# Kernel optimization log

Hardware: AMD Instinct MI355X
Metric: run time of the kernel (lower is better)

Reference implementation:

```python
import jax, jax.numpy as jnp
import numpy as np

EMBED_DIM = 1024
N_HEADS = 16
HEAD_DIM = EMBED_DIM // N_HEADS


def setup_inputs() -> dict:
    key = jax.random.key(0)
    k_x, k_wi, k_bi, k_wo, k_bo = jax.random.split(key, 5)
    B, N, C = 4, 2048, EMBED_DIM
    scale = 1.0 / np.sqrt(C)
    return {
        "x": jax.random.normal(k_x, (B, N, C), dtype=jnp.float32),
        "w_in": jax.random.normal(k_wi, (C, 3 * C), dtype=jnp.float32) * scale,
        "b_in": jax.random.normal(k_bi, (3 * C,), dtype=jnp.float32) * 0.01,
        "w_out": jax.random.normal(k_wo, (C, C), dtype=jnp.float32) * scale,
        "b_out": jax.random.normal(k_bo, (C,), dtype=jnp.float32) * 0.01,
    }


def reference(x, w_in, b_in, w_out, b_out):
    B, N, C = x.shape
    H, D = N_HEADS, HEAD_DIM
    qkv = x @ w_in + b_in  # (B, N, 3C)
    q, k, v = jnp.split(qkv, 3, axis=-1)
    # (B, H, N, D)
    q = q.reshape(B, N, H, D).transpose(0, 2, 1, 3)
    k = k.reshape(B, N, H, D).transpose(0, 2, 1, 3)
    v = v.reshape(B, N, H, D).transpose(0, 2, 1, 3)
    # Naive attention: full (B,H,N,N) scores, NO sqrt(d) scaling (as in source)
    scores = jnp.einsum("bhnd,bhmd->bhnm", q, k)
    attn = jax.nn.softmax(scores, axis=-1)
    out = jnp.einsum("bhnm,bhmd->bhnd", attn, v)
    out = out.transpose(0, 2, 1, 3).reshape(B, N, C)
    return out @ w_out + b_out
```

## Files before the change

### kernel.cpp

```cpp
#include <hip/hip_runtime.h>
#include <hip/hip_bf16.h>
#include <stdint.h>

typedef __attribute__((ext_vector_type(8))) __bf16 bf8v;
typedef __attribute__((ext_vector_type(4))) float f4v;

#define L2E 1.44269504088896f

__device__ __forceinline__ unsigned short f2bf(float f) {
  union { float f; unsigned u; } v; v.f = f;
  unsigned r = v.u + 0x7fffu + ((v.u >> 16) & 1u);
  return (unsigned short)(r >> 16);
}

__device__ __forceinline__ unsigned pk2bf(float f0, float f1) {
  union { __hip_bfloat162 h; unsigned u; } c;
  c.h = __float22bfloat162_rn(make_float2(f0, f1));
  return c.u;
}

__device__ __forceinline__ float exp2_hw(float x) {
  return __builtin_amdgcn_exp2f(x);
}

__device__ __forceinline__ void gl_lds16(const void* g, void* l) {
  __builtin_amdgcn_global_load_lds(
      (__attribute__((address_space(1))) void*)(g),
      (__attribute__((address_space(3))) void*)(l), 16, 0, 0);
}

__global__ void cast_bf16_kernel(const float* __restrict__ in,
                                 unsigned short* __restrict__ out) {
  int i = blockIdx.x * 256 + threadIdx.x;
  float4 v = ((const float4*)in)[i];
  ushort4 o;
  o.x = f2bf(v.x); o.y = f2bf(v.y); o.z = f2bf(v.z); o.w = f2bf(v.w);
  ((ushort4*)out)[i] = o;
}

__global__ void transpose_w_kernel(const float* __restrict__ w_in,
                                   const float* __restrict__ w_out,
                                   unsigned short* __restrict__ wiT,
                                   unsigned short* __restrict__ woT) {
  __shared__ float tile[32][33];
  int bx = blockIdx.x;
  const float* in; unsigned short* out; int C, c0;
  if (bx < 96) { in = w_in;  out = wiT; C = 3072; c0 = bx * 32; }
  else         { in = w_out; out = woT; C = 1024; c0 = (bx - 96) * 32; }
  int r0 = blockIdx.y * 32;
  int tx = threadIdx.x, ty = threadIdx.y;
#pragma unroll
  for (int j = 0; j < 4; ++j)
    tile[ty + 8 * j][tx] = in[(size_t)(r0 + ty + 8 * j) * C + c0 + tx];
  __syncthreads();
#pragma unroll
  for (int j = 0; j < 4; ++j)
    out[(size_t)(c0 + ty + 8 * j) * 1024 + r0 + tx] = f2bf(tile[tx][ty + 8 * j]);
}

__global__ void transpose_v_kernel(const unsigned short* __restrict__ qkv,
                                   unsigned short* __restrict__ vtg) {
  __shared__ unsigned short tile[32][33];
  int bh = blockIdx.z;
  int d0 = blockIdx.y * 32;
  int n0 = blockIdx.x * 32;
  int b = bh >> 4, h = bh & 15;
  int tx = threadIdx.x, ty = threadIdx.y;
  const unsigned short* src = qkv + (size_t)b * 2048 * 3072 + 2048 + h * 64 + d0;
#pragma unroll
  for (int j = 0; j < 4; ++j)
    tile[ty + 8 * j][tx] = src[(size_t)(n0 + ty + 8 * j) * 3072 + tx];
  __syncthreads();
  unsigned short* dst = vtg + ((size_t)bh * 64) * 2048;
#pragma unroll
  for (int j = 0; j < 4; ++j)
    dst[(size_t)(d0 + ty + 8 * j) * 2048 + n0 + tx] = tile[tx][ty + 8 * j];
}

__global__ __launch_bounds__(256, 2) void gemm_bt(
    const unsigned short* __restrict__ A,
    const unsigned short* __restrict__ BT,
    const float* __restrict__ bias,
    unsigned short* __restrict__ C,
    int M, int N, int K, int scale_ncols, float scale) {
  __shared__ __align__(16) unsigned short As[128 * 32];
  __shared__ __align__(16) unsigned short Bs[128 * 32];
  const int tid = threadIdx.x;
  const int wave = tid >> 6, lane = tid & 63;
  const int lo = lane & 15, hi = lane >> 4;
  const int m0 = blockIdx.y * 128, n0 = blockIdx.x * 128;
  const int wm = (wave >> 1) * 64, wn = (wave & 1) * 64;

  f4v acc[4][4] = {};

  const int srow = lane >> 2;
  const int scol = (lane & 3) * 8;

  for (int k0 = 0; k0 < K; k0 += 32) {
#pragma unroll
    for (int p = 0; p < 2; ++p) {
      int r = p * 64 + wave * 16 + srow;
      gl_lds16(A + (size_t)(m0 + r) * K + k0 + scol,
               &As[(p * 64 + wave * 16) * 32]);
      gl_lds16(BT + (size_t)(n0 + r) * K + k0 + scol,
               &Bs[(p * 64 + wave * 16) * 32]);
    }
    __syncthreads();
    bf8v a[4], b[4];
#pragma unroll
    for (int i = 0; i < 4; ++i)
      a[i] = *(const bf8v*)&As[(wm + i * 16 + lo) * 32 + hi * 8];
#pragma unroll
    for (int j = 0; j < 4; ++j)
      b[j] = *(const bf8v*)&Bs[(wn + j * 16 + lo) * 32 + hi * 8];
#pragma unroll
    for (int i = 0; i < 4; ++i)
#pragma unroll
      for (int j = 0; j < 4; ++j)
        acc[i][j] = __builtin_amdgcn_mfma_f32_16x16x32_bf16(a[i], b[j], acc[i][j], 0, 0, 0);
    __syncthreads();
  }

#pragma unroll
  for (int i = 0; i < 4; ++i) {
#pragma unroll
    for (int r = 0; r < 4; ++r) {
      int row = m0 + wm + i * 16 + hi * 4 + r;
#pragma unroll
      for (int j = 0; j < 4; ++j) {
        int col = n0 + wn + j * 16 + lo;
        float v = acc[i][j][r] + bias[col];
        if (col < scale_ncols) v *= scale;
        C[(size_t)row * N + col] = f2bf(v);
      }
    }
  }
}

__global__ __launch_bounds__(256, 4) void gemm_bt_sm(
    const unsigned short* __restrict__ A,
    const unsigned short* __restrict__ BT,
    const float* __restrict__ bias,
    float* __restrict__ C,
    int M, int N, int K) {
  __shared__ __align__(16) unsigned short As[64 * 32];
  __shared__ __align__(16) unsigned short Bs[128 * 32];
  const int tid = threadIdx.x;
  const int wave = tid >> 6, lane = tid & 63;
  const int lo = lane & 15, hi = lane >> 4;
  const int m0 = blockIdx.y * 64, n0 = blockIdx.x * 128;
  const int wm = (wave >> 1) * 32, wn = (wave & 1) * 64;

  f4v acc[2][4] = {};

  const int srow = lane >> 2;
  const int scol = (lane & 3) * 8;

  for (int k0 = 0; k0 < K; k0 += 32) {
    gl_lds16(A + (size_t)(m0 + wave * 16 + srow) * K + k0 + scol,
             &As[(wave * 16) * 32]);
#pragma unroll
    for (int p = 0; p < 2; ++p) {
      int r = p * 64 + wave * 16 + srow;
      gl_lds16(BT + (size_t)(n0 + r) * K + k0 + scol,
               &Bs[(p * 64 + wave * 16) * 32]);
    }
    __syncthreads();
    bf8v a[2], b[4];
#pragma unroll
    for (int i = 0; i < 2; ++i)
      a[i] = *(const bf8v*)&As[(wm + i * 16 + lo) * 32 + hi * 8];
#pragma unroll
    for (int j = 0; j < 4; ++j)
      b[j] = *(const bf8v*)&Bs[(wn + j * 16 + lo) * 32 + hi * 8];
#pragma unroll
    for (int i = 0; i < 2; ++i)
#pragma unroll
      for (int j = 0; j < 4; ++j)
        acc[i][j] = __builtin_amdgcn_mfma_f32_16x16x32_bf16(a[i], b[j], acc[i][j], 0, 0, 0);
    __syncthreads();
  }

#pragma unroll
  for (int i = 0; i < 2; ++i) {
#pragma unroll
    for (int r = 0; r < 4; ++r) {
      int row = m0 + wm + i * 16 + hi * 4 + r;
#pragma unroll
      for (int j = 0; j < 4; ++j) {
        int col = n0 + wn + j * 16 + lo;
        C[(size_t)row * N + col] = acc[i][j][r] + bias[col];
      }
    }
  }
}

#define FSTR 72

__global__ __launch_bounds__(256, 4) void flash_attn(
    const unsigned short* __restrict__ qkv,
    const unsigned short* __restrict__ vtg,
    unsigned short* __restrict__ y) {
  __shared__ __align__(16) unsigned short Ps[128 * FSTR];
  __shared__ __align__(16) unsigned short Kt[64 * FSTR];
  __shared__ __align__(16) unsigned short Vt[64 * FSTR];
  const int tid = threadIdx.x;
  const int wave = tid >> 6, lane = tid & 63;
  const int lo = lane & 15, hi = lane >> 4;
  const int b = blockIdx.z, h = blockIdx.y, q0 = blockIdx.x * 128;
  const size_t base = (size_t)b * 2048 * 3072;
  const int qoff = h * 64, koff = 1024 + h * 64;
  const unsigned short* vsrc = vtg + (size_t)(b * 16 + h) * 64 * 2048;

#pragma unroll
  for (int i = 0; i < 4; ++i) {
    int cid = i * 256 + tid;
    int m = cid >> 3, c = cid & 7;
    *(float4*)&Ps[m * FSTR + c * 8] =
        *(const float4*)(qkv + base + (size_t)(q0 + m) * 3072 + qoff + c * 8);
  }
  __syncthreads();
  bf8v bq[2][2];
#pragma unroll
  for (int qt = 0; qt < 2; ++qt)
#pragma unroll
    for (int ks = 0; ks < 2; ++ks)
      bq[qt][ks] = *(const bf8v*)&Ps[(wave * 32 + qt * 16 + lo) * FSTR + ks * 32 + hi * 8];
  __syncthreads();

  f4v O[2][4] = {};
  float l_st[2] = {0.f, 0.f};

  for (int kt = 0; kt < 32; ++kt) {
    const int mb = kt * 64;
#pragma unroll
    for (int i = 0; i < 2; ++i) {
      int cid = i * 256 + tid;
      int m = cid >> 3, c = cid & 7;
      *(float4*)&Kt[m * FSTR + c * 8] =
          *(const float4*)(qkv + base + (size_t)(mb + m) * 3072 + koff + c * 8);
      *(float4*)&Vt[m * FSTR + c * 8] =
          *(const float4*)(vsrc + (size_t)m * 2048 + mb + c * 8);
    }
    __syncthreads();

    f4v s2[4][2] = {};
#pragma unroll
    for (int ks = 0; ks < 2; ++ks) {
#pragma unroll
      for (int ct = 0; ct < 4; ++ct) {
        bf8v ak = *(const bf8v*)&Kt[(ct * 16 + lo) * FSTR + ks * 32 + hi * 8];
        s2[ct][0] = __builtin_amdgcn_mfma_f32_16x16x32_bf16(ak, bq[0][ks], s2[ct][0], 0, 0, 0);
        s2[ct][1] = __builtin_amdgcn_mfma_f32_16x16x32_bf16(ak, bq[1][ks], s2[ct][1], 0, 0, 0);
      }
    }

#pragma unroll
    for (int qt = 0; qt < 2; ++qt) {
      int prow = (wave * 32 + qt * 16 + lo) * FSTR;
#pragma unroll
      for (int ct = 0; ct < 4; ++ct) {
        float p0 = exp2_hw(s2[ct][qt][0]);
        float p1 = exp2_hw(s2[ct][qt][1]);
        float p2 = exp2_hw(s2[ct][qt][2]);
        float p3 = exp2_hw(s2[ct][qt][3]);
        l_st[qt] += (p0 + p1) + (p2 + p3);
        uint2 w;
        w.x = pk2bf(p0, p1);
        w.y = pk2bf(p2, p3);
        *(uint2*)&Ps[prow + ct * 16 + hi * 4] = w;
      }
    }

#pragma unroll
    for (int ks = 0; ks < 2; ++ks) {
      bf8v ap0 = *(const bf8v*)&Ps[(wave * 32 + lo) * FSTR + ks * 32 + hi * 8];
      bf8v ap1 = *(const bf8v*)&Ps[(wave * 32 + 16 + lo) * FSTR + ks * 32 + hi * 8];
#pragma unroll
      for (int dt = 0; dt < 4; ++dt) {
        bf8v bv = *(const bf8v*)&Vt[(dt * 16 + lo) * FSTR + ks * 32 + hi * 8];
        O[0][dt] = __builtin_amdgcn_mfma_f32_16x16x32_bf16(ap0, bv, O[0][dt], 0, 0, 0);
        O[1][dt] = __builtin_amdgcn_mfma_f32_16x16x32_bf16(ap1, bv, O[1][dt], 0, 0, 0);
      }
    }
    __syncthreads();
  }

#pragma unroll
  for (int qt = 0; qt < 2; ++qt) {
    float lt = l_st[qt];
    lt += __shfl_xor(lt, 16);
    lt += __shfl_xor(lt, 32);
    l_st[qt] = lt;
  }
#pragma unroll
  for (int qt = 0; qt < 2; ++qt) {
#pragma unroll
    for (int r = 0; r < 4; ++r) {
      float lr = __shfl(l_st[qt], hi * 4 + r);
      float inv = 1.f / lr;
      int row = q0 + wave * 32 + qt * 16 + hi * 4 + r;
      size_t orow = ((size_t)b * 2048 + row) * 1024 + h * 64;
#pragma unroll
      for (int dt = 0; dt < 4; ++dt)
        y[orow + dt * 16 + lo] = f2bf(O[qt][dt][r] * inv);
    }
  }
}

extern "C" void kernel_launch(void* const* d_in, const int* in_sizes, int n_in,
                              void* d_out, int out_size, void* d_ws, size_t ws_size,
                              hipStream_t stream) {
  (void)in_sizes; (void)n_in; (void)out_size; (void)ws_size;
  const float* x     = (const float*)d_in[0];
  const float* w_in  = (const float*)d_in[1];
  const float* b_in  = (const float*)d_in[2];
  const float* w_out = (const float*)d_in[3];
  const float* b_out = (const float*)d_in[4];

  unsigned short* xb  = (unsigned short*)d_ws;
  unsigned short* wiT = xb  + (size_t)8192 * 1024;
  unsigned short* woT = wiT + (size_t)3072 * 1024;
  unsigned short* qkv = woT + (size_t)1024 * 1024;
  unsigned short* yb  = qkv + (size_t)8192 * 3072;
  unsigned short* vtg = xb;

  cast_bf16_kernel<<<8192, 256, 0, stream>>>(x, xb);
  transpose_w_kernel<<<dim3(128, 32), dim3(32, 8), 0, stream>>>(w_in, w_out, wiT, woT);

  gemm_bt<<<dim3(24, 64), 256, 0, stream>>>(xb, wiT, b_in, qkv, 8192, 3072, 1024,
                                            1024, L2E);
  transpose_v_kernel<<<dim3(64, 2, 64), dim3(32, 8), 0, stream>>>(qkv, vtg);
  flash_attn<<<dim3(16, 16, 4), 256, 0, stream>>>(qkv, vtg, yb);
  gemm_bt_sm<<<dim3(8, 128), 256, 0, stream>>>(yb, woT, b_out, (float*)d_out,
                                               8192, 1024, 1024);
}
```

Before: 305.5 us.

## Prefetch K/V tiles into registers, compute row sums via MFMA, swizzle block order

Each K/V tile is now loaded from global memory into registers one iteration ahead and written to shared memory at the start of the next iteration, so global latency overlaps with compute. The softmax denominator is computed by an extra MFMA against a vector of ones on the bf16 P tile, which replaces the scalar sums and shuffle reductions. Block indices are remapped with a swizzle to change L2 locality, and s_setprio is raised around the MFMA sections. The cost is extra register pressure and a denominator summed from bf16-rounded probabilities, which now matches the P values actually used in the PV product.

```diff
diff --git a/kernel.cpp b/kernel.cpp
--- a/kernel.cpp
+++ b/kernel.cpp
@@ -207,10 +207,35 @@
   const int tid = threadIdx.x;
   const int wave = tid >> 6, lane = tid & 63;
   const int lo = lane & 15, hi = lane >> 4;
-  const int b = blockIdx.z, h = blockIdx.y, q0 = blockIdx.x * 128;
+
+  const int lin = (((blockIdx.z << 4) | blockIdx.y) << 4) | blockIdx.x;
+  const int swz = (lin & 7) * 128 + (lin >> 3);
+  const int q0 = (swz & 15) << 7;
+  const int h  = (swz >> 4) & 15;
+  const int b  = swz >> 8;
+
   const size_t base = (size_t)b * 2048 * 3072;
   const int qoff = h * 64, koff = 1024 + h * 64;
   const unsigned short* vsrc = vtg + (size_t)(b * 16 + h) * 64 * 2048;
+
+  const int m_st = tid >> 3, c_st = tid & 7;
+  const unsigned short* kg = qkv + base + koff;
+  float4 rk0, rk1, rv0, rv1;
+  auto kv_load = [&](int kt) {
+    const int mb = kt * 64;
+    rk0 = *(const float4*)(kg + (size_t)(mb + m_st) * 3072 + c_st * 8);
+    rk1 = *(const float4*)(kg + (size_t)(mb + m_st + 32) * 3072 + c_st * 8);
+    rv0 = *(const float4*)(vsrc + (size_t)m_st * 2048 + mb + c_st * 8);
+    rv1 = *(const float4*)(vsrc + (size_t)(m_st + 32) * 2048 + mb + c_st * 8);
+  };
+  auto kv_write = [&]() {
+    *(float4*)&Kt[m_st * FSTR + c_st * 8] = rk0;
+    *(float4*)&Kt[(m_st + 32) * FSTR + c_st * 8] = rk1;
+    *(float4*)&Vt[m_st * FSTR + c_st * 8] = rv0;
+    *(float4*)&Vt[(m_st + 32) * FSTR + c_st * 8] = rv1;
+  };
+
+  kv_load(0);
 
 #pragma unroll
   for (int i = 0; i < 4; ++i) {
@@ -226,49 +251,46 @@
 #pragma unroll
     for (int ks = 0; ks < 2; ++ks)
       bq[qt][ks] = *(const bf8v*)&Ps[(wave * 32 + qt * 16 + lo) * FSTR + ks * 32 + hi * 8];
-  __syncthreads();
 
   f4v O[2][4] = {};
-  float l_st[2] = {0.f, 0.f};
+  f4v acc_l[2] = {};
+  union { bf8v v; unsigned short u[8]; } onesu;
+#pragma unroll
+  for (int i = 0; i < 8; ++i) onesu.u[i] = 0x3F80;
+  const bf8v ones = onesu.v;
 
   for (int kt = 0; kt < 32; ++kt) {
-    const int mb = kt * 64;
-#pragma unroll
-    for (int i = 0; i < 2; ++i) {
-      int cid = i * 256 + tid;
-      int m = cid >> 3, c = cid & 7;
-      *(float4*)&Kt[m * FSTR + c * 8] =
-          *(const float4*)(qkv + base + (size_t)(mb + m) * 3072 + koff + c * 8);
-      *(float4*)&Vt[m * FSTR + c * 8] =
-          *(const float4*)(vsrc + (size_t)m * 2048 + mb + c * 8);
-    }
-    __syncthreads();
-
-    f4v s2[4][2] = {};
-#pragma unroll
-    for (int ks = 0; ks < 2; ++ks) {
-#pragma unroll
-      for (int ct = 0; ct < 4; ++ct) {
+    asm volatile("" ::: "memory");
+    __builtin_amdgcn_s_barrier();
+    asm volatile("" ::: "memory");
+    kv_write();
+    if (kt < 31) kv_load(kt + 1);
+    asm volatile("s_waitcnt lgkmcnt(0)" ::: "memory");
+    __builtin_amdgcn_s_barrier();
+    asm volatile("" ::: "memory");
+
+#pragma unroll
+    for (int ct = 0; ct < 4; ++ct) {
+      f4v s0 = {}, s1 = {};
+      __builtin_amdgcn_s_setprio(1);
+#pragma unroll
+      for (int ks = 0; ks < 2; ++ks) {
         bf8v ak = *(const bf8v*)&Kt[(ct * 16 + lo) * FSTR + ks * 32 + hi * 8];
-        s2[ct][0] = __builtin_amdgcn_mfma_f32_16x16x32_bf16(ak, bq[0][ks], s2[ct][0], 0, 0, 0);
-        s2[ct][1] = __builtin_amdgcn_mfma_f32_16x16x32_bf16(ak, bq[1][ks], s2[ct][1], 0, 0, 0);
-      }
-    }
-
-#pragma unroll
-    for (int qt = 0; qt < 2; ++qt) {
-      int prow = (wave * 32 + qt * 16 + lo) * FSTR;
-#pragma unroll
-      for (int ct = 0; ct < 4; ++ct) {
-        float p0 = exp2_hw(s2[ct][qt][0]);
-        float p1 = exp2_hw(s2[ct][qt][1]);
-        float p2 = exp2_hw(s2[ct][qt][2]);
-        float p3 = exp2_hw(s2[ct][qt][3]);
-        l_st[qt] += (p0 + p1) + (p2 + p3);
-        uint2 w;
-        w.x = pk2bf(p0, p1);
-        w.y = pk2bf(p2, p3);
-        *(uint2*)&Ps[prow + ct * 16 + hi * 4] = w;
+        s0 = __builtin_amdgcn_mfma_f32_16x16x32_bf16(ak, bq[0][ks], s0, 0, 0, 0);
+        s1 = __builtin_amdgcn_mfma_f32_16x16x32_bf16(ak, bq[1][ks], s1, 0, 0, 0);
+      }
+      __builtin_amdgcn_s_setprio(0);
+      {
+        float p0 = exp2_hw(s0[0]), p1 = exp2_hw(s0[1]);
+        float p2 = exp2_hw(s0[2]), p3 = exp2_hw(s0[3]);
+        uint2 w; w.x = pk2bf(p0, p1); w.y = pk2bf(p2, p3);
+        *(uint2*)&Ps[(wave * 32 + lo) * FSTR + ct * 16 + hi * 4] = w;
+      }
+      {
+        float p0 = exp2_hw(s1[0]), p1 = exp2_hw(s1[1]);
+        float p2 = exp2_hw(s1[2]), p3 = exp2_hw(s1[3]);
+        uint2 w; w.x = pk2bf(p0, p1); w.y = pk2bf(p2, p3);
+        *(uint2*)&Ps[(wave * 32 + 16 + lo) * FSTR + ct * 16 + hi * 4] = w;
       }
     }
 
@@ -276,29 +298,24 @@
     for (int ks = 0; ks < 2; ++ks) {
       bf8v ap0 = *(const bf8v*)&Ps[(wave * 32 + lo) * FSTR + ks * 32 + hi * 8];
       bf8v ap1 = *(const bf8v*)&Ps[(wave * 32 + 16 + lo) * FSTR + ks * 32 + hi * 8];
+      __builtin_amdgcn_s_setprio(1);
+      acc_l[0] = __builtin_amdgcn_mfma_f32_16x16x32_bf16(ap0, ones, acc_l[0], 0, 0, 0);
+      acc_l[1] = __builtin_amdgcn_mfma_f32_16x16x32_bf16(ap1, ones, acc_l[1], 0, 0, 0);
 #pragma unroll
       for (int dt = 0; dt < 4; ++dt) {
         bf8v bv = *(const bf8v*)&Vt[(dt * 16 + lo) * FSTR + ks * 32 + hi * 8];
         O[0][dt] = __builtin_amdgcn_mfma_f32_16x16x32_bf16(ap0, bv, O[0][dt], 0, 0, 0);
         O[1][dt] = __builtin_amdgcn_mfma_f32_16x16x32_bf16(ap1, bv, O[1][dt], 0, 0, 0);
       }
-    }
-    __syncthreads();
+      __builtin_amdgcn_s_setprio(0);
+    }
   }
 
 #pragma unroll
   for (int qt = 0; qt < 2; ++qt) {
-    float lt = l_st[qt];
-    lt += __shfl_xor(lt, 16);
-    lt += __shfl_xor(lt, 32);
-    l_st[qt] = lt;
-  }
-#pragma unroll
-  for (int qt = 0; qt < 2; ++qt) {
 #pragma unroll
     for (int r = 0; r < 4; ++r) {
-      float lr = __shfl(l_st[qt], hi * 4 + r);
-      float inv = 1.f / lr;
+      float inv = 1.f / acc_l[qt][r];
       int row = q0 + wave * 32 + qt * 16 + hi * 4 + r;
       size_t orow = ((size_t)b * 2048 + row) * 1024 + h * 64;
 #pragma unroll
```

Result: no change. 303.8 us (-0.6%).
